# Kernel tuning notes

Measured on AMD Instinct MI355X. Metric: run time of the kernel, lower is better.

Reference implementation:

```python
import jax, jax.numpy as jnp
import numpy as np

RES = (256, 256, 256)
CH = 16
RR = 8  # ceil(log2(256))
N_PTS = 262144


def grid_sample_2d(plane, gx, gy):
    """Bilinear grid_sample, align_corners=True.
    plane: (C, H, W); gx in [-1,1] indexes W, gy indexes H. Returns (N, C)."""
    C, H, W = plane.shape
    ix = (gx + 1.0) * 0.5 * (W - 1)
    iy = (gy + 1.0) * 0.5 * (H - 1)
    x0f = jnp.floor(ix)
    y0f = jnp.floor(iy)
    wx = ix - x0f
    wy = iy - y0f
    x0 = jnp.clip(x0f.astype(jnp.int32), 0, W - 1)
    x1 = jnp.clip(x0 + 1, 0, W - 1)
    y0 = jnp.clip(y0f.astype(jnp.int32), 0, H - 1)
    y1 = jnp.clip(y0 + 1, 0, H - 1)
    v00 = plane[:, y0, x0]  # (C, N)
    v01 = plane[:, y0, x1]
    v10 = plane[:, y1, x0]
    v11 = plane[:, y1, x1]
    out = (v00 * (1 - wx) * (1 - wy) + v01 * wx * (1 - wy)
           + v10 * (1 - wx) * wy + v11 * wx * wy)
    return out.T  # (N, C)


def integrate(P, coords):
    """P: (N, 2*CH, RR) with real part channels [:CH], imag [CH:].
    coords: (N,) in [-1,1]. Fourier-basis numerical integration (real part)."""
    c = (coords + 1.0) * 0.5 * (2 ** RR - 1)  # (N,)
    coef = jnp.concatenate([jnp.zeros((1,), jnp.float32),
                            2.0 ** jnp.arange(RR - 1, dtype=jnp.float32)]) / (2 ** RR)
    theta = 2.0 * jnp.pi * c[:, None] * coef  # (N, RR)
    # Re(exp(i*theta) . P_complex) = cos.Re(P) - sin.Im(P)
    re = jnp.einsum('nr,ncr->nc', jnp.cos(theta), P[:, :CH, :])
    im = jnp.einsum('nr,ncr->nc', jnp.sin(theta), P[:, CH:, :])
    return re - im  # (N, CH)


def setup_inputs() -> dict:
    key = jax.random.key(0)
    k0, k1, k2, k3 = jax.random.split(key, 4)
    inputs = jax.random.uniform(k0, (N_PTS, 3), dtype=jnp.float32,
                                minval=-1.0, maxval=1.0)
    C = 2 * RR * CH
    Pu = 0.001 * jax.random.normal(k1, (1, C, RES[1], RES[2]), dtype=jnp.float32)
    Pv = 0.001 * jax.random.normal(k2, (1, C, RES[0], RES[2]), dtype=jnp.float32)
    Pw = 0.001 * jax.random.normal(k3, (1, C, RES[0], RES[1]), dtype=jnp.float32)
    return {"inputs": inputs, "Pu": Pu, "Pv": Pv, "Pw": Pw}


def reference(inputs, Pu, Pv, Pw):
    c0, c1, c2 = inputs[:, 0], inputs[:, 1], inputs[:, 2]
    # grid last-dim (x,y): x indexes width (last plane axis), y the height.
    su = grid_sample_2d(Pu[0], c1, c2).reshape(-1, 2 * CH, RR)
    sv = grid_sample_2d(Pv[0], c0, c2).reshape(-1, 2 * CH, RR)
    sw = grid_sample_2d(Pw[0], c0, c1).reshape(-1, 2 * CH, RR)
    return integrate(su, c0) + integrate(sv, c1) + integrate(sw, c2)  # (N, CH)
```

## Files before the change

### kernel.cpp

```cpp
#include <hip/hip_runtime.h>
#include <hip/hip_fp16.h>
#include <math.h>

#define NPTS 262144
#define PLANE_ELEMS 16777216u

typedef __attribute__((ext_vector_type(4))) float f4;
typedef __attribute__((ext_vector_type(8))) unsigned short us8;
typedef __attribute__((ext_vector_type(4))) unsigned int u4;

#define OFF_SORTED   (3ull * PLANE_ELEMS * 2ull)
#define OFF_PARTIAL  (OFF_SORTED + (size_t)3 * NPTS * 16)
#define OFF_HIST     (OFF_PARTIAL + (size_t)3 * NPTS * 16 * 2)
#define WS_NEED      (OFF_HIST + (size_t)3 * 65536 * 4)

__device__ __forceinline__ void plane_xy(int p, float c0, float c1, float c2,
                                         float& gx, float& gy, float& ax) {
  if (p == 0)      { gx = c1; gy = c2; ax = c0; }
  else if (p == 1) { gx = c0; gy = c2; ax = c1; }
  else             { gx = c0; gy = c1; ax = c2; }
}

__device__ __forceinline__ int cell_of(float g) {
  float i = (g + 1.f) * 0.5f * 255.f;
  int x0 = (int)floorf(i);
  return x0 < 0 ? 0 : (x0 > 255 ? 255 : x0);
}

__global__ __launch_bounds__(256) void PREFFFT_trans_k(
    const float* __restrict__ Pu, const float* __restrict__ Pv,
    const float* __restrict__ Pw, __half* __restrict__ dst0) {
  __shared__ float tile[64][65];
  const float* src = blockIdx.z == 0 ? Pu : (blockIdx.z == 1 ? Pv : Pw);
  __half* dst = dst0 + (size_t)blockIdx.z * PLANE_ELEMS;
  unsigned hw0 = blockIdx.x * 64u;
  unsigned c0  = blockIdx.y * 64u;
  int tid = threadIdx.x;
  int lr = tid >> 4, lc = tid & 15;
#pragma unroll
  for (int j = 0; j < 4; ++j) {
    int r = lr + j * 16;
    f4 v = *(const f4*)(src + (size_t)(c0 + r) * 65536u + hw0 + lc * 4);
    tile[r][lc * 4 + 0] = v.x; tile[r][lc * 4 + 1] = v.y;
    tile[r][lc * 4 + 2] = v.z; tile[r][lc * 4 + 3] = v.w;
  }
  __syncthreads();
  int wr = tid >> 3, ws = tid & 7;
#pragma unroll
  for (int j = 0; j < 2; ++j) {
    int row = wr + j * 32;
    __half2 h[4];
#pragma unroll
    for (int k = 0; k < 4; ++k)
      h[k] = __floats2half2_rn(tile[ws * 8 + 2 * k][row],
                               tile[ws * 8 + 2 * k + 1][row]);
    *(us8*)(dst + (size_t)(hw0 + row) * 256u + c0 + ws * 8) = *(us8*)h;
  }
}

__global__ __launch_bounds__(256) void PREFFFT_hist_k(
    const float* __restrict__ inputs, unsigned* __restrict__ hist) {
  int n = blockIdx.x * 256 + threadIdx.x;
  if (n >= NPTS) return;
  float c0 = inputs[n * 3 + 0], c1 = inputs[n * 3 + 1], c2 = inputs[n * 3 + 2];
#pragma unroll
  for (int p = 0; p < 3; ++p) {
    float gx, gy, ax;
    plane_xy(p, c0, c1, c2, gx, gy, ax);
    int key = (cell_of(gy) << 8) | cell_of(gx);
    atomicAdd(&hist[p * 65536 + key], 1u);
  }
}

__global__ __launch_bounds__(1024) void PREFFFT_scan_k(unsigned* __restrict__ hist) {
  __shared__ unsigned part[1024];
  unsigned* h = hist + (size_t)blockIdx.x * 65536;
  int t = threadIdx.x;
  unsigned s = 0;
#pragma unroll 8
  for (int i = 0; i < 64; ++i) s += h[t * 64 + i];
  part[t] = s;
  __syncthreads();
  for (int off = 1; off < 1024; off <<= 1) {
    unsigned v = (t >= off) ? part[t - off] : 0u;
    __syncthreads();
    part[t] += v;
    __syncthreads();
  }
  unsigned run = (t == 0) ? 0u : part[t - 1];
#pragma unroll 8
  for (int i = 0; i < 64; ++i) {
    unsigned c = h[t * 64 + i];
    h[t * 64 + i] = run;
    run += c;
  }
}

__global__ __launch_bounds__(256) void PREFFFT_scat_k(
    const float* __restrict__ inputs, unsigned* __restrict__ hist,
    float4* __restrict__ sortedC) {
  int n = blockIdx.x * 256 + threadIdx.x;
  if (n >= NPTS) return;
  float c0 = inputs[n * 3 + 0], c1 = inputs[n * 3 + 1], c2 = inputs[n * 3 + 2];
#pragma unroll
  for (int p = 0; p < 3; ++p) {
    float gx, gy, ax;
    plane_xy(p, c0, c1, c2, gx, gy, ax);
    int key = (cell_of(gy) << 8) | cell_of(gx);
    unsigned pos = atomicAdd(&hist[p * 65536 + key], 1u);
    sortedC[(size_t)p * NPTS + pos] =
        make_float4(c0, c1, c2, __uint_as_float((unsigned)n));
  }
}

__global__ __launch_bounds__(256) void PREFFFT_samp_k(
    const float4* __restrict__ sortedC, const __half* __restrict__ T,
    __half* __restrict__ partial) {
  int p = blockIdx.y;
  int bx = blockIdx.x;
  int lbx = (bx & 7) * 1024 + (bx >> 3);
  int slot = lbx * 32 + ((int)threadIdx.x >> 3);
  int t = threadIdx.x & 7;

  float4 sc = sortedC[(size_t)p * NPTS + slot];
  unsigned n = __float_as_uint(sc.w);
  float gx, gy, ax;
  plane_xy(p, sc.x, sc.y, sc.z, gx, gy, ax);

  float ix = (gx + 1.f) * 0.5f * 255.f;
  float iy = (gy + 1.f) * 0.5f * 255.f;
  float x0f = floorf(ix), y0f = floorf(iy);
  float wx = ix - x0f, wy = iy - y0f;
  int x0 = (int)x0f; x0 = x0 < 0 ? 0 : (x0 > 255 ? 255 : x0);
  int y0 = (int)y0f; y0 = y0 < 0 ? 0 : (y0 > 255 ? 255 : y0);
  int x1 = x0 + 1 > 255 ? 255 : x0 + 1;
  int y1 = y0 + 1 > 255 ? 255 : y0 + 1;
  float w00 = (1.f - wx) * (1.f - wy);
  float w01 = wx * (1.f - wy);
  float w10 = (1.f - wx) * wy;
  float w11 = wx * wy;

  const __half* __restrict__ P = T + (size_t)p * PLANE_ELEMS;
  int r00 = (y0 * 256 + x0) * 256, r01 = (y0 * 256 + x1) * 256;
  int r10 = (y1 * 256 + x0) * 256, r11 = (y1 * 256 + x1) * 256;
  int ore = t * 16;
  int oim = 128 + t * 16;

  f4 a0 = *(const f4*)(P + r00 + ore),     a1 = *(const f4*)(P + r00 + ore + 8);
  f4 a2 = *(const f4*)(P + r00 + oim),     a3 = *(const f4*)(P + r00 + oim + 8);
  f4 b0 = *(const f4*)(P + r01 + ore),     b1 = *(const f4*)(P + r01 + ore + 8);
  f4 b2 = *(const f4*)(P + r01 + oim),     b3 = *(const f4*)(P + r01 + oim + 8);
  f4 c0v = *(const f4*)(P + r10 + ore),    c1v = *(const f4*)(P + r10 + ore + 8);
  f4 c2v = *(const f4*)(P + r10 + oim),    c3v = *(const f4*)(P + r10 + oim + 8);
  f4 d0 = *(const f4*)(P + r11 + ore),     d1 = *(const f4*)(P + r11 + ore + 8);
  f4 d2 = *(const f4*)(P + r11 + oim),     d3 = *(const f4*)(P + r11 + oim + 8);

  __half2 hw00 = __float2half2_rn(w00), hw01 = __float2half2_rn(w01);
  __half2 hw10 = __float2half2_rn(w10), hw11 = __float2half2_rn(w11);

  __half2 bre[8], bim[8];
#pragma unroll
  for (int q = 0; q < 4; ++q) {
    const __half2* pa;
    pa = (const __half2*)&a0;  __half2 v;
    v = __hmul2(pa[q], hw00);
    v = __hfma2(((const __half2*)&b0)[q],  hw01, v);
    v = __hfma2(((const __half2*)&c0v)[q], hw10, v);
    bre[q] = __hfma2(((const __half2*)&d0)[q], hw11, v);

    v = __hmul2(((const __half2*)&a1)[q], hw00);
    v = __hfma2(((const __half2*)&b1)[q],  hw01, v);
    v = __hfma2(((const __half2*)&c1v)[q], hw10, v);
    bre[q + 4] = __hfma2(((const __half2*)&d1)[q], hw11, v);

    v = __hmul2(((const __half2*)&a2)[q], hw00);
    v = __hfma2(((const __half2*)&b2)[q],  hw01, v);
    v = __hfma2(((const __half2*)&c2v)[q], hw10, v);
    bim[q] = __hfma2(((const __half2*)&d2)[q], hw11, v);

    v = __hmul2(((const __half2*)&a3)[q], hw00);
    v = __hfma2(((const __half2*)&b3)[q],  hw01, v);
    v = __hfma2(((const __half2*)&c3v)[q], hw10, v);
    bim[q + 4] = __hfma2(((const __half2*)&d3)[q], hw11, v);
  }

  float fre[16], fim[16];
#pragma unroll
  for (int q = 0; q < 8; ++q) {
    float2 vr = __half22float2(bre[q]);
    float2 vi = __half22float2(bim[q]);
    fre[2 * q] = vr.x; fre[2 * q + 1] = vr.y;
    fim[2 * q] = vi.x; fim[2 * q + 1] = vi.y;
  }

  float cs = (ax + 1.f) * 0.5f * 255.f;
  float th = 6.283185307179586f * cs * (1.f / 256.f);
  float s, c;
  __sincosf(th, &s, &c);
  float aR0 = fre[0], aR1 = fre[8];
  float aI0 = 0.f,    aI1 = 0.f;
#pragma unroll
  for (int r = 1; r < 8; ++r) {
    aR0 += fre[r] * c;     aR1 += fre[8 + r] * c;
    aI0 += fim[r] * s;     aI1 += fim[8 + r] * s;
    if (r < 7) {
      float c2 = c + c;
      float cn = c2 * c - 1.f;
      s = c2 * s;
      c = cn;
    }
  }

  *(__half2*)(partial + ((size_t)p * NPTS + n) * 16 + 2 * t) =
      __floats2half2_rn(aR0 - aI0, aR1 - aI1);
}

__global__ __launch_bounds__(256) void PREFFFT_red_k(
    const __half* __restrict__ part, float* __restrict__ out) {
  size_t i = (size_t)blockIdx.x * 256 + threadIdx.x;
  const size_t PS = (size_t)NPTS * 16;
  union H8 { u4 v; __half2 h[4]; };
  H8 a, b, c;
  a.v = *(const u4*)(part + i * 8);
  b.v = *(const u4*)(part + PS + i * 8);
  c.v = *(const u4*)(part + 2 * PS + i * 8);
  f4 o0, o1;
#pragma unroll
  for (int k = 0; k < 4; ++k) {
    float2 fa = __half22float2(a.h[k]);
    float2 fb = __half22float2(b.h[k]);
    float2 fc = __half22float2(c.h[k]);
    float lo = fa.x + fb.x + fc.x;
    float hi = fa.y + fb.y + fc.y;
    if (k < 2) { o0[2 * k] = lo; o0[2 * k + 1] = hi; }
    else       { o1[2 * (k - 2)] = lo; o1[2 * (k - 2) + 1] = hi; }
  }
  ((f4*)out)[i * 2] = o0;
  ((f4*)out)[i * 2 + 1] = o1;
}

__global__ __launch_bounds__(256) void PREFFFT_fallback_k(
    const float* __restrict__ inputs, const float* __restrict__ Tu,
    const float* __restrict__ Tv, const float* __restrict__ Tw,
    float* __restrict__ out) {
  int gtid = blockIdx.x * 256 + threadIdx.x;
  int n = gtid >> 5;
  int t = threadIdx.x & 31;
  const bool is_re = t < 16;
  float c0 = inputs[n * 3 + 0], c1 = inputs[n * 3 + 1], c2 = inputs[n * 3 + 2];
  const float* PL[3] = {Tu, Tv, Tw};
  float acc = 0.f;
#pragma unroll
  for (int p = 0; p < 3; ++p) {
    float gx, gy, ax;
    plane_xy(p, c0, c1, c2, gx, gy, ax);
    float ix = (gx + 1.f) * 0.5f * 255.f;
    float iy = (gy + 1.f) * 0.5f * 255.f;
    float x0f = floorf(ix), y0f = floorf(iy);
    float wx = ix - x0f, wy = iy - y0f;
    int x0 = (int)x0f; x0 = x0 < 0 ? 0 : (x0 > 255 ? 255 : x0);
    int y0 = (int)y0f; y0 = y0 < 0 ? 0 : (y0 > 255 ? 255 : y0);
    int x1 = x0 + 1 > 255 ? 255 : x0 + 1;
    int y1 = y0 + 1 > 255 ? 255 : y0 + 1;
    float w00 = (1.f - wx) * (1.f - wy), w01 = wx * (1.f - wy);
    float w10 = (1.f - wx) * wy, w11 = wx * wy;
    int i00 = y0 * 256 + x0, i01 = y0 * 256 + x1;
    int i10 = y1 * 256 + x0, i11 = y1 * 256 + x1;
    float b[8];
#pragma unroll
    for (int j = 0; j < 8; ++j) {
      const float* base = PL[p] + (size_t)(t * 8 + j) * 65536u;
      b[j] = w00 * base[i00] + w01 * base[i01] + w10 * base[i10] + w11 * base[i11];
    }
    float csv = (ax + 1.f) * 0.5f * 255.f;
    float theta1 = 6.283185307179586f * csv * (1.f / 256.f);
    float partial = is_re ? b[0] : 0.f;
#pragma unroll
    for (int r = 1; r < 8; ++r) {
      float thr = theta1 * (float)(1 << (r - 1));
      float s, c;
      __sincosf(thr, &s, &c);
      partial += b[r] * (is_re ? c : s);
    }
    float other = __shfl_xor(partial, 16);
    acc += partial - other;
  }
  if (is_re) out[n * 16 + t] = acc;
}

extern "C" void kernel_launch(void* const* d_in, const int* in_sizes, int n_in,
                              void* d_out, int out_size, void* d_ws, size_t ws_size,
                              hipStream_t stream) {
  const float* inputs = (const float*)d_in[0];
  const float* Pu = (const float*)d_in[1];
  const float* Pv = (const float*)d_in[2];
  const float* Pw = (const float*)d_in[3];
  float* out = (float*)d_out;

  if (ws_size >= WS_NEED) {
    char* ws = (char*)d_ws;
    __half*   T       = (__half*)ws;
    float4*   sortedC = (float4*)(ws + OFF_SORTED);
    __half*   partial = (__half*)(ws + OFF_PARTIAL);
    unsigned* hist    = (unsigned*)(ws + OFF_HIST);

    {
      dim3 tg(1024, 4, 3);
      PREFFFT_trans_k<<<tg, 256, 0, stream>>>(Pu, Pv, Pw, T);
    }
    hipMemsetAsync(hist, 0, (size_t)3 * 65536 * 4, stream);
    PREFFFT_hist_k<<<NPTS / 256, 256, 0, stream>>>(inputs, hist);
    PREFFFT_scan_k<<<3, 1024, 0, stream>>>(hist);
    PREFFFT_scat_k<<<NPTS / 256, 256, 0, stream>>>(inputs, hist, sortedC);
    {
      dim3 tg(NPTS / 32, 3);
      PREFFFT_samp_k<<<tg, 256, 0, stream>>>(sortedC, T, partial);
    }
    PREFFFT_red_k<<<2048, 256, 0, stream>>>(partial, out);
  } else {
    PREFFFT_fallback_k<<<NPTS / 8, 256, 0, stream>>>(inputs, Pu, Pv, Pw, out);
  }
}
```

Before: 234.0 us.

## Store half-precision planes channel-group-major and transpose without shared memory

```diff
diff --git a/kernel.cpp b/kernel.cpp
--- a/kernel.cpp
+++ b/kernel.cpp
@@ -6,7 +6,6 @@
 #define PLANE_ELEMS 16777216u
 
 typedef __attribute__((ext_vector_type(4))) float f4;
-typedef __attribute__((ext_vector_type(8))) unsigned short us8;
 typedef __attribute__((ext_vector_type(4))) unsigned int u4;
 
 #define OFF_SORTED   (3ull * PLANE_ELEMS * 2ull)
@@ -30,31 +29,30 @@
 __global__ __launch_bounds__(256) void PREFFFT_trans_k(
     const float* __restrict__ Pu, const float* __restrict__ Pv,
     const float* __restrict__ Pw, __half* __restrict__ dst0) {
-  __shared__ float tile[64][65];
   const float* src = blockIdx.z == 0 ? Pu : (blockIdx.z == 1 ? Pv : Pw);
   __half* dst = dst0 + (size_t)blockIdx.z * PLANE_ELEMS;
-  unsigned hw0 = blockIdx.x * 64u;
-  unsigned c0  = blockIdx.y * 64u;
-  int tid = threadIdx.x;
-  int lr = tid >> 4, lc = tid & 15;
-#pragma unroll
-  for (int j = 0; j < 4; ++j) {
-    int r = lr + j * 16;
-    f4 v = *(const f4*)(src + (size_t)(c0 + r) * 65536u + hw0 + lc * 4);
-    tile[r][lc * 4 + 0] = v.x; tile[r][lc * 4 + 1] = v.y;
-    tile[r][lc * 4 + 2] = v.z; tile[r][lc * 4 + 3] = v.w;
-  }
-  __syncthreads();
-  int wr = tid >> 3, ws = tid & 7;
-#pragma unroll
-  for (int j = 0; j < 2; ++j) {
-    int row = wr + j * 32;
-    __half2 h[4];
-#pragma unroll
-    for (int k = 0; k < 4; ++k)
-      h[k] = __floats2half2_rn(tile[ws * 8 + 2 * k][row],
-                               tile[ws * 8 + 2 * k + 1][row]);
-    *(us8*)(dst + (size_t)(hw0 + row) * 256u + c0 + ws * 8) = *(us8*)h;
+  const unsigned c_hi = blockIdx.y;
+  const unsigned hw = blockIdx.x * 1024u + threadIdx.x * 4u;
+
+  const float* base = src + (size_t)(c_hi * 16u) * 65536u + hw;
+  f4 v[16];
+#pragma unroll
+  for (int i = 0; i < 16; ++i)
+    v[i] = *(const f4*)(base + (size_t)i * 65536u);
+
+  __half* d = dst + (size_t)c_hi * 1048576u + (size_t)hw * 16u;
+#pragma unroll
+  for (int k = 0; k < 4; ++k) {
+    unsigned w[8];
+#pragma unroll
+    for (int j = 0; j < 8; ++j) {
+      __half2 h = __floats2half2_rn(v[2 * j][k], v[2 * j + 1][k]);
+      w[j] = *(unsigned*)&h;
+    }
+    u4 lo{w[0], w[1], w[2], w[3]};
+    u4 hi{w[4], w[5], w[6], w[7]};
+    *(u4*)(d + k * 16) = lo;
+    *(u4*)(d + k * 16 + 8) = hi;
   }
 }
 
@@ -140,20 +138,20 @@
   float w10 = (1.f - wx) * wy;
   float w11 = wx * wy;
 
-  const __half* __restrict__ P = T + (size_t)p * PLANE_ELEMS;
-  int r00 = (y0 * 256 + x0) * 256, r01 = (y0 * 256 + x1) * 256;
-  int r10 = (y1 * 256 + x0) * 256, r11 = (y1 * 256 + x1) * 256;
-  int ore = t * 16;
-  int oim = 128 + t * 16;
-
-  f4 a0 = *(const f4*)(P + r00 + ore),     a1 = *(const f4*)(P + r00 + ore + 8);
-  f4 a2 = *(const f4*)(P + r00 + oim),     a3 = *(const f4*)(P + r00 + oim + 8);
-  f4 b0 = *(const f4*)(P + r01 + ore),     b1 = *(const f4*)(P + r01 + ore + 8);
-  f4 b2 = *(const f4*)(P + r01 + oim),     b3 = *(const f4*)(P + r01 + oim + 8);
-  f4 c0v = *(const f4*)(P + r10 + ore),    c1v = *(const f4*)(P + r10 + ore + 8);
-  f4 c2v = *(const f4*)(P + r10 + oim),    c3v = *(const f4*)(P + r10 + oim + 8);
-  f4 d0 = *(const f4*)(P + r11 + ore),     d1 = *(const f4*)(P + r11 + ore + 8);
-  f4 d2 = *(const f4*)(P + r11 + oim),     d3 = *(const f4*)(P + r11 + oim + 8);
+  const __half* __restrict__ Pre =
+      T + (size_t)p * PLANE_ELEMS + (size_t)t * 1048576u;
+  const __half* __restrict__ Pim = Pre + 8u * 1048576u;
+  int r00 = (y0 * 256 + x0) * 16, r01 = (y0 * 256 + x1) * 16;
+  int r10 = (y1 * 256 + x0) * 16, r11 = (y1 * 256 + x1) * 16;
+
+  f4 a0 = *(const f4*)(Pre + r00),   a1 = *(const f4*)(Pre + r00 + 8);
+  f4 a2 = *(const f4*)(Pim + r00),   a3 = *(const f4*)(Pim + r00 + 8);
+  f4 b0 = *(const f4*)(Pre + r01),   b1 = *(const f4*)(Pre + r01 + 8);
+  f4 b2 = *(const f4*)(Pim + r01),   b3 = *(const f4*)(Pim + r01 + 8);
+  f4 c0v = *(const f4*)(Pre + r10),  c1v = *(const f4*)(Pre + r10 + 8);
+  f4 c2v = *(const f4*)(Pim + r10),  c3v = *(const f4*)(Pim + r10 + 8);
+  f4 d0 = *(const f4*)(Pre + r11),   d1 = *(const f4*)(Pre + r11 + 8);
+  f4 d2 = *(const f4*)(Pim + r11),   d3 = *(const f4*)(Pim + r11 + 8);
 
   __half2 hw00 = __float2half2_rn(w00), hw01 = __float2half2_rn(w01);
   __half2 hw10 = __float2half2_rn(w10), hw11 = __float2half2_rn(w11);
@@ -161,9 +159,8 @@
   __half2 bre[8], bim[8];
 #pragma unroll
   for (int q = 0; q < 4; ++q) {
-    const __half2* pa;
-    pa = (const __half2*)&a0;  __half2 v;
-    v = __hmul2(pa[q], hw00);
+    __half2 v;
+    v = __hmul2(((const __half2*)&a0)[q], hw00);
     v = __hfma2(((const __half2*)&b0)[q],  hw01, v);
     v = __hfma2(((const __half2*)&c0v)[q], hw10, v);
     bre[q] = __hfma2(((const __half2*)&d0)[q], hw11, v);
@@ -305,7 +302,7 @@
     unsigned* hist    = (unsigned*)(ws + OFF_HIST);
 
     {
-      dim3 tg(1024, 4, 3);
+      dim3 tg(64, 16, 3);
       PREFFFT_trans_k<<<tg, 256, 0, stream>>>(Pu, Pv, Pw, T);
     }
     hipMemsetAsync(hist, 0, (size_t)3 * 65536 * 4, stream);
```

Result: slower. 372.9 us (+59.4%).
